# Kernel tuning notes

Hardware: AMD Instinct MI355X
Metric: run time of the kernel (lower is better)

Reference implementation:

```python
import jax, jax.numpy as jnp
import numpy as np

N = 100000   # nodes
E = 300000   # edges (avg degree ~3, molecular graphs)
DIN = 128    # input node features
H = 512      # hidden
OUT = 256    # out_channels
G = 4096     # number of graphs
EPS = 1e-5
SLOPE = 0.01  # LeakyReLU default negative slope
SELF_W = 2.0  # improved=True self-loop weight


def setup_inputs() -> dict:
    key = jax.random.key(0)
    ks = jax.random.split(key, 12)
    x = jax.random.normal(ks[0], (N, DIN), dtype=jnp.float32)
    edge_index = jax.random.randint(ks[1], (2, E), 0, N, dtype=jnp.int64)
    batch = jnp.sort(jax.random.randint(ks[2], (N,), 0, G, dtype=jnp.int64))
    s1 = 1.0 / np.sqrt(DIN)
    s2 = 1.0 / np.sqrt(H)
    return {
        "x": x,
        "edge_index": edge_index,
        "batch": batch,
        "W1": jax.random.normal(ks[3], (DIN, H), dtype=jnp.float32) * s1,
        "b1": jax.random.normal(ks[4], (H,), dtype=jnp.float32) * 0.01,
        "g1": jax.random.uniform(ks[5], (H,), dtype=jnp.float32, minval=0.5, maxval=1.5),
        "beta1": jax.random.normal(ks[6], (H,), dtype=jnp.float32) * 0.01,
        "W2": jax.random.normal(ks[7], (H, H), dtype=jnp.float32) * s2,
        "b2": jax.random.normal(ks[8], (H,), dtype=jnp.float32) * 0.01,
        "g2": jax.random.uniform(ks[9], (H,), dtype=jnp.float32, minval=0.5, maxval=1.5),
        "beta2": jax.random.normal(ks[10], (H,), dtype=jnp.float32) * 0.01,
        "Wf": jax.random.normal(ks[11], (H, OUT), dtype=jnp.float32) * s2,
        "bf": jnp.zeros((OUT,), dtype=jnp.float32),
    }


def _gcn_conv(x, W, b, row, col, n):
    # GCNConv(improved=True, add_self_loops=True, normalize=True), edge_weight=None
    h = x @ W                                   # [n, H]
    ones = jnp.ones(row.shape[0], dtype=h.dtype)
    deg = jax.ops.segment_sum(ones, col, num_segments=n) + SELF_W
    dinv = jax.lax.rsqrt(deg)                   # deg > 0 always (self-loop weight 2)
    norm = dinv[row] * dinv[col]                # [E]
    agg = jax.ops.segment_sum(h[row] * norm[:, None], col, num_segments=n)
    agg = agg + h * (SELF_W * dinv * dinv)[:, None]  # self-loop messages, no edge materialization
    return agg + b


def _bn(x, g, beta):
    # training-mode BatchNorm1d: biased batch stats
    mu = jnp.mean(x, axis=0)
    var = jnp.mean(jnp.square(x - mu), axis=0)
    return g * (x - mu) * jax.lax.rsqrt(var + EPS) + beta


def reference(x, edge_index, batch, W1, b1, g1, beta1, W2, b2, g2, beta2, Wf, bf):
    row, col = edge_index[0], edge_index[1]
    n = x.shape[0]
    h = _gcn_conv(x, W1, b1, row, col, n)
    h = jax.nn.leaky_relu(_bn(h, g1, beta1), SLOPE)
    # dropout is identity in eval mode
    h = _gcn_conv(h, W2, b2, row, col, n)
    h = jax.nn.leaky_relu(_bn(h, g2, beta2), SLOPE)
    pooled = jax.ops.segment_max(h, batch, num_segments=G)
    pooled = jnp.where(jnp.isfinite(pooled), pooled, 0.0)  # empty graphs -> 0 (torch_scatter fill)
    return pooled @ Wf + bf
```

## Files before the change

### kernel.cpp

```cpp
#include <hip/hip_runtime.h>
#include <hip/hip_bf16.h>

typedef __hip_bfloat16 bf16;
typedef __attribute__((ext_vector_type(8))) short short8;
typedef __attribute__((ext_vector_type(4))) float f32x4;

#define HDIM 512
#define SLOPE 0.01f
#define BN_EPS 1e-5f
#define STRIPES 8

__device__ inline float bf2f(short s) {
    unsigned u = ((unsigned)(unsigned short)s) << 16;
    return __builtin_bit_cast(float, u);
}
__device__ inline unsigned short f2bfbits(float v) {
    bf16 h = __float2bfloat16(v);
    return (unsigned short)__builtin_bit_cast(short, h);
}

struct EdgeRec { int src; float nm; };

__global__ void detect_types(const int* __restrict__ ei, const unsigned* __restrict__ xw,
                             int* __restrict__ flags, float* __restrict__ gpart) {
    __shared__ int nzhi, okbf;
    if (threadIdx.x == 0) { nzhi = 0; okbf = 0; }
    __syncthreads();
    int lo = 0, ok = 0;
    for (int i = threadIdx.x; i < 2048; i += 256)
        if (ei[2 * i + 1] != 0) lo++;
    for (int i = threadIdx.x; i < 1024; i += 256) {
        unsigned w = (xw[i] & 0xFFFFu) << 16;
        float av = fabsf(__builtin_bit_cast(float, w));
        if (av > 0.0009f && av < 64.0f) ok++;
    }
    for (int i = threadIdx.x; i < STRIPES * 2 * HDIM; i += 256) gpart[i] = 0.f;
    if (lo) atomicAdd(&nzhi, lo);
    if (ok) atomicAdd(&okbf, ok);
    __syncthreads();
    if (threadIdx.x == 0) {
        flags[0] = (nzhi == 0) ? 1 : 0;
        flags[1] = (okbf < 512) ? 1 : 0;
    }
}

__global__ void conv_all_idx(const int* __restrict__ ei, const int* __restrict__ batch,
                             int* __restrict__ ei32, int* __restrict__ batch32,
                             int* __restrict__ cnt, int e2, int n,
                             const int* __restrict__ flags) {
    int i = blockIdx.x * blockDim.x + threadIdx.x;
    int i64 = flags[0];
    if (i < e2) {
        int v = i64 ? (int)((const long long*)ei)[i] : ei[i];
        ei32[i] = v;
        if (i >= e2 / 2) atomicAdd(&cnt[v], 1);
    } else if (i < e2 + n) {
        int j = i - e2;
        batch32[j] = i64 ? (int)((const long long*)batch)[j] : batch[j];
    }
}

__global__ void wt_conv_all(const void* __restrict__ W1, const void* __restrict__ W2,
                            const void* __restrict__ Wf, const void* __restrict__ bf_,
                            bf16* __restrict__ W1T, bf16* __restrict__ W2T,
                            bf16* __restrict__ WfT, bf16* __restrict__ bfbf,
                            const int* __restrict__ flags) {
    const int S1 = 128 * 512, S2 = 512 * 512, S3 = 512 * 256;
    int idx = blockIdx.x * 256 + threadIdx.x;
    bool f32 = flags[1] != 0;
    if (idx < S1) {
        int nn = idx / 128, k = idx - nn * 128;
        float v = f32 ? ((const float*)W1)[(size_t)k * 512 + nn]
                      : __bfloat162float(((const bf16*)W1)[(size_t)k * 512 + nn]);
        W1T[idx] = __float2bfloat16(v);
    } else if (idx < S1 + S2) {
        int t = idx - S1;
        int nn = t / 512, k = t - nn * 512;
        float v = f32 ? ((const float*)W2)[(size_t)k * 512 + nn]
                      : __bfloat162float(((const bf16*)W2)[(size_t)k * 512 + nn]);
        W2T[t] = __float2bfloat16(v);
    } else if (idx < S1 + S2 + S3) {
        int t = idx - S1 - S2;
        int nn = t / 512, k = t - nn * 512;
        float v = f32 ? ((const float*)Wf)[(size_t)k * 256 + nn]
                      : __bfloat162float(((const bf16*)Wf)[(size_t)k * 256 + nn]);
        WfT[t] = __float2bfloat16(v);
    } else if (idx < S1 + S2 + S3 + 256) {
        int t = idx - S1 - S2 - S3;
        float v = f32 ? ((const float*)bf_)[t]
                      : __bfloat162float(((const bf16*)bf_)[t]);
        bfbf[t] = __float2bfloat16(v);
    }
}

__global__ __launch_bounds__(256) void scan_part(
    const int* __restrict__ counts, int* __restrict__ offsets,
    int* __restrict__ bsum, float* __restrict__ dinv, float* __restrict__ selfw,
    int n)
{
    __shared__ int s[512];
    int b = blockIdx.x;
    int base = b * 512;
    int t = threadIdx.x;
    int c0 = (base + t       < n) ? counts[base + t]       : 0;
    int c1 = (base + t + 256 < n) ? counts[base + t + 256] : 0;
    s[t] = c0; s[t + 256] = c1;
    if (base + t < n) {
        float d = (float)c0 + 2.0f;
        dinv[base + t] = rsqrtf(d);
        selfw[base + t] = 2.0f / d;
    }
    if (base + t + 256 < n) {
        float d = (float)c1 + 2.0f;
        dinv[base + t + 256] = rsqrtf(d);
        selfw[base + t + 256] = 2.0f / d;
    }

    int offset = 1;
    for (int d = 256; d > 0; d >>= 1) {
        __syncthreads();
        if (t < d) {
            int ai = offset * (2 * t + 1) - 1;
            int bi = offset * (2 * t + 2) - 1;
            s[bi] += s[ai];
        }
        offset <<= 1;
    }
    __syncthreads();
    if (t == 0) { bsum[b] = s[511]; s[511] = 0; }
    for (int d = 1; d < 512; d <<= 1) {
        offset >>= 1;
        __syncthreads();
        if (t < d) {
            int ai = offset * (2 * t + 1) - 1;
            int bi = offset * (2 * t + 2) - 1;
            int tmp = s[ai]; s[ai] = s[bi]; s[bi] += tmp;
        }
    }
    __syncthreads();
    if (base + t < n)       offsets[base + t]       = s[t];
    if (base + t + 256 < n) offsets[base + t + 256] = s[t + 256];
}

__global__ __launch_bounds__(1024) void scan_tops(int* __restrict__ bsum, int nb) {
    __shared__ int s[1024];
    int t = threadIdx.x;
    s[t] = (t < nb) ? bsum[t] : 0;
    __syncthreads();
    for (int off = 1; off < 1024; off <<= 1) {
        int v = (t >= off) ? s[t - off] : 0;
        __syncthreads();
        s[t] += v;
        __syncthreads();
    }
    if (t < nb) bsum[t] = (t == 0) ? 0 : s[t - 1];
}

__global__ __launch_bounds__(256) void scan_add(
    int* __restrict__ offsets, const int* __restrict__ bsum, int n, int e)
{
    int b = blockIdx.x;
    int base = b * 512;
    int add = bsum[b];
    int t = threadIdx.x;
    if (base + t < n)       offsets[base + t]       += add;
    if (base + t + 256 < n) offsets[base + t + 256] += add;
    if (b == 0 && t == 0) offsets[n] = e;
}

__global__ void scatter_edges(const int* __restrict__ rows, const int* __restrict__ cols,
                              const int* __restrict__ offsets, int* __restrict__ cursor,
                              const float* __restrict__ dinv,
                              EdgeRec* __restrict__ er, int e)
{
    int i = blockIdx.x * blockDim.x + threadIdx.x;
    if (i < e) {
        int d = cols[i];
        int r = rows[i];
        int pos = offsets[d] + atomicAdd(&cursor[d], 1);
        EdgeRec rec;
        rec.src = r;
        rec.nm = dinv[d] * dinv[r];
        er[pos] = rec;
    }
}

#define GEMM_STAGE(boff, kk)                                                             \
    {                                                                                    \
        _Pragma("unroll")                                                                \
        for (int i_ = 0; i_ < 2; i_++) {                                                 \
            int c_ = wave * 2 + i_;                                                      \
            const bf16* ga_ = A  + (size_t)(m0 + c_ * 16 + lrow) * K + (kk) + lcol;      \
            const bf16* gb_ = BT + (size_t)(n0 + c_ * 16 + lrow) * K + (kk) + lcol;      \
            __builtin_amdgcn_global_load_lds(                                            \
                (const __attribute__((address_space(1))) unsigned*)ga_,                  \
                (__attribute__((address_space(3))) unsigned*)(smem + (boff) + c_ * 512), \
                16, 0, 0);                                                               \
            __builtin_amdgcn_global_load_lds(                                            \
                (const __attribute__((address_space(1))) unsigned*)gb_,                  \
                (__attribute__((address_space(3))) unsigned*)(smem + 8192 + (boff) + c_ * 512), \
                16, 0, 0);                                                               \
        }                                                                                \
    }

#define GEMM_COMPUTE(boff)                                                               \
    {                                                                                    \
        short8 a[4], b[4];                                                               \
        _Pragma("unroll")                                                                \
        for (int mi2 = 0; mi2 < 4; mi2++)                                                \
            a[mi2] = *(const short8*)&smem[(boff) + (wm + mi2 * 16 + r) * 32 + aoff];    \
        _Pragma("unroll")                                                                \
        for (int ni = 0; ni < 4; ni++)                                                   \
            b[ni] = *(const short8*)&smem[8192 + (boff) + (wn + ni * 16 + r) * 32 + aoff]; \
        _Pragma("unroll")                                                                \
        for (int mi2 = 0; mi2 < 4; mi2++)                                                \
            _Pragma("unroll")                                                            \
            for (int ni = 0; ni < 4; ni++)                                               \
                acc[mi2][ni] = __builtin_amdgcn_mfma_f32_16x16x32_bf16(                  \
                    a[mi2], b[ni], acc[mi2][ni], 0, 0, 0);                               \
    }

template<bool STATS>
__global__ __launch_bounds__(256, 4) void gemm_m97(
    const bf16* __restrict__ A, const bf16* __restrict__ BT,
    void* __restrict__ C, const bf16* __restrict__ bias,
    int M, int K, int N, const int* __restrict__ cf32,
    float* __restrict__ gpart, int MB)
{
    __shared__ bf16 smem[16384];

    int NBN = N >> 7;
    int id = blockIdx.x;
    int grp = id / (8 * NBN);
    int loc = id - grp * 8 * NBN;
    int mi = loc & 7;
    int nblk = loc >> 3;
    int mblk = grp * 8 + mi;
    if (mblk >= MB) return;

    int tid = threadIdx.x;
    int wave = tid >> 6, lane = tid & 63, q = lane >> 4, r = lane & 15;
    int wm = (wave >> 1) * 64, wn = (wave & 1) * 64;
    int m0 = mblk * 128, n0 = nblk * 128;
    bool c32 = cf32 && *cf32;

    int lrow = lane >> 2;
    int lcol = (((lane & 3) ^ ((lane >> 3) & 3)) * 8);
    int aoff = (q ^ ((r >> 1) & 3)) * 8;

    f32x4 acc[4][4];
#pragma unroll
    for (int mi2 = 0; mi2 < 4; mi2++)
#pragma unroll
        for (int ni = 0; ni < 4; ni++)
            acc[mi2][ni] = {0.f, 0.f, 0.f, 0.f};

    const int nK = K >> 5;

    GEMM_STAGE(0, 0);

    int cur = 0;
    for (int t = 1; t < nK; ++t) {
        GEMM_STAGE(cur ^ 4096, t * 32);
        asm volatile("s_waitcnt vmcnt(4)" ::: "memory");
        __builtin_amdgcn_sched_barrier(0);
        __builtin_amdgcn_s_barrier();
        __builtin_amdgcn_sched_barrier(0);
        GEMM_COMPUTE(cur);
        asm volatile("s_waitcnt lgkmcnt(0)" ::: "memory");
        __builtin_amdgcn_sched_barrier(0);
        __builtin_amdgcn_s_barrier();
        __builtin_amdgcn_sched_barrier(0);
        cur ^= 4096;
    }
    asm volatile("s_waitcnt vmcnt(0)" ::: "memory");
    __builtin_amdgcn_sched_barrier(0);
    __builtin_amdgcn_s_barrier();
    __builtin_amdgcn_sched_barrier(0);
    GEMM_COMPUTE(cur);

    if (!c32) {
        __syncthreads();
#pragma unroll
        for (int mi2 = 0; mi2 < 4; mi2++) {
#pragma unroll
            for (int ni = 0; ni < 4; ni++) {
                int lc = wn + ni * 16 + r;
                float bv = bias ? __bfloat162float(bias[n0 + lc]) : 0.f;
#pragma unroll
                for (int reg = 0; reg < 4; reg++) {
                    int lr = wm + mi2 * 16 + q * 4 + reg;
                    int bo = ((lr << 8) + (lc << 1)) ^ (q << 5);
                    *(bf16*)((char*)smem + bo) = __float2bfloat16(acc[mi2][ni][reg] + bv);
                }
            }
        }
        __syncthreads();
#pragma unroll
        for (int pss = 0; pss < 8; pss++) {
            int off = pss * 4096 + tid * 16;
            int row = off >> 8;
            int cb = off & 255;
            int rb = cb ^ (((row >> 2) & 3) << 5);
            f32x4 v = *(const f32x4*)((const char*)smem + (row << 8) + rb);
            int gm = m0 + row;
            if (gm < M)
                *(f32x4*)((char*)C + (((size_t)gm * N + n0) << 1) + cb) = v;
        }
    } else {
#pragma unroll
        for (int mi2 = 0; mi2 < 4; mi2++) {
#pragma unroll
            for (int ni = 0; ni < 4; ni++) {
                int gn = n0 + wn + ni * 16 + r;
                float bv = bias ? __bfloat162float(bias[gn]) : 0.f;
#pragma unroll
                for (int reg = 0; reg < 4; reg++) {
                    int gm = m0 + wm + mi2 * 16 + q * 4 + reg;
                    if (gm < M)
                        ((float*)C)[(size_t)gm * N + gn] = acc[mi2][ni][reg] + bv;
                }
            }
        }
    }

    if constexpr (STATS) {
        float* base = gpart + (size_t)(mblk & (STRIPES - 1)) * 2 * HDIM;
#pragma unroll
        for (int ni = 0; ni < 4; ni++) {
            float cs = 0.f, cq = 0.f;
#pragma unroll
            for (int mi2 = 0; mi2 < 4; mi2++)
#pragma unroll
                for (int reg = 0; reg < 4; reg++) {
                    int gm = m0 + wm + mi2 * 16 + q * 4 + reg;
                    if (gm < M) {
                        float v = acc[mi2][ni][reg];
                        cs += v; cq += v * v;
                    }
                }
            cs += __shfl_xor(cs, 16, 64);
            cs += __shfl_xor(cs, 32, 64);
            cq += __shfl_xor(cq, 16, 64);
            cq += __shfl_xor(cq, 32, 64);
            if (q == 0) {
                int c = n0 + wn + ni * 16 + r;
                atomicAdd(&base[c], cs);
                atomicAdd(&base[HDIM + c], cq);
            }
        }
    }
}

#define AGG_DIN_BODY(LOADV)                                                            \
    int dst = gw;                                                                      \
    if (dst < n) {                                                                     \
        int s0 = offsets[dst], s1 = offsets[dst + 1];                                  \
        float sw = selfw[dst];                                                         \
        float h0, h1; LOADV(dst, h0, h1);                                              \
        while (dst < n) {                                                              \
            int nd = dst + nw;                                                         \
            int ns0 = 0, ns1 = 0; float nsw = 0.f, nh0 = 0.f, nh1 = 0.f;               \
            if (nd < n) {                                                              \
                ns0 = offsets[nd]; ns1 = offsets[nd + 1]; nsw = selfw[nd];             \
                LOADV(nd, nh0, nh1);                                                   \
            }                                                                          \
            float a0 = sw * h0, a1 = sw * h1;                                          \
            int p = s0;                                                                \
            for (; p + 3 < s1; p += 4) {                                               \
                EdgeRec e0 = er[p], e1 = er[p + 1], e2 = er[p + 2], e3 = er[p + 3];    \
                float x0, y0, x1, y1, x2, y2, x3, y3;                                  \
                LOADV(e0.src, x0, y0); LOADV(e1.src, x1, y1);                          \
                LOADV(e2.src, x2, y2); LOADV(e3.src, x3, y3);                          \
                a0 += e0.nm * x0 + e1.nm * x1 + e2.nm * x2 + e3.nm * x3;               \
                a1 += e0.nm * y0 + e1.nm * y1 + e2.nm * y2 + e3.nm * y3;               \
            }                                                                          \
            int rem = s1 - p;                                                          \
            if (rem > 0) {                                                             \
                EdgeRec e0 = er[p], e1 = e0, e2 = e0;                                  \
                if (rem > 1) e1 = er[p + 1];                                           \
                if (rem > 2) e2 = er[p + 2];                                           \
                float x0, y0, x1 = 0.f, y1 = 0.f, x2 = 0.f, y2 = 0.f;                  \
                LOADV(e0.src, x0, y0);                                                 \
                if (rem > 1) LOADV(e1.src, x1, y1);                                    \
                if (rem > 2) LOADV(e2.src, x2, y2);                                    \
                a0 += e0.nm * x0; a1 += e0.nm * y0;                                    \
                if (rem > 1) { a0 += e1.nm * x1; a1 += e1.nm * y1; }                   \
                if (rem > 2) { a0 += e2.nm * x2; a1 += e2.nm * y2; }                   \
            }                                                                          \
            ((unsigned*)out)[(size_t)dst * 64 + lane] =                                \
                (unsigned)f2bfbits(a0) | ((unsigned)f2bfbits(a1) << 16);               \
            dst = nd; s0 = ns0; s1 = ns1; sw = nsw; h0 = nh0; h1 = nh1;                \
        }                                                                              \
    }

#define LOADF32(idx, a, b) { float2 v_ = ((const float2*)x)[(size_t)(idx) * 64 + lane]; \
                             a = v_.x; b = v_.y; }
#define LOADBF(idx, a, b)  { unsigned u_ = ((const unsigned*)x)[(size_t)(idx) * 64 + lane]; \
                             a = bf2f((short)(u_ & 0xFFFF)); b = bf2f((short)(u_ >> 16)); }

__global__ __launch_bounds__(256) void agg_csr_din(
    const void* __restrict__ x, const int* __restrict__ offsets,
    const EdgeRec* __restrict__ er, const float* __restrict__ selfw,
    bf16* __restrict__ out, int n, const int* __restrict__ flags)
{
    int wave = threadIdx.x >> 6, lane = threadIdx.x & 63;
    int gw = blockIdx.x * 4 + wave;
    int nw = gridDim.x * 4;
    bool f32 = flags[1] != 0;
    if (f32) { AGG_DIN_BODY(LOADF32) } else { AGG_DIN_BODY(LOADBF) }
}

__device__ inline void bnlk8(const short8& v, const float* sc, const float* sh,
                             float* t) {
#pragma unroll
    for (int j = 0; j < 8; j++) {
        float u = sc[j] * bf2f(v[j]) + sh[j];
        t[j] = u > 0.f ? u : SLOPE * u;
    }
}

__global__ __launch_bounds__(256) void agg_csr_bn(
    const bf16* __restrict__ h, const int* __restrict__ offsets,
    const EdgeRec* __restrict__ er, const float* __restrict__ selfw,
    const float* __restrict__ scale, const float* __restrict__ shift,
    bf16* __restrict__ y, int n)
{
    int wave = threadIdx.x >> 6, lane = threadIdx.x & 63;
    int f0 = lane * 8;
    int gw = blockIdx.x * 4 + wave;
    int nw = gridDim.x * 4;

    float sc[8], sh[8];
#pragma unroll
    for (int j = 0; j < 8; j++) { sc[j] = scale[f0 + j]; sh[j] = shift[f0 + j]; }

    int dst = gw;
    if (dst >= n) return;
    int s0 = offsets[dst], s1 = offsets[dst + 1];
    float sw = selfw[dst];
    short8 hv = *(const short8*)(h + (size_t)dst * HDIM + f0);

    while (dst < n) {
        int nd = dst + nw;
        int ns0 = 0, ns1 = 0; float nsw = 0.f; short8 nhv = {};
        if (nd < n) {
            ns0 = offsets[nd]; ns1 = offsets[nd + 1]; nsw = selfw[nd];
            nhv = *(const short8*)(h + (size_t)nd * HDIM + f0);
        }

        float acc[8], t[8];
        bnlk8(hv, sc, sh, t);
#pragma unroll
        for (int j = 0; j < 8; j++) acc[j] = sw * t[j];

        int p = s0;
        for (; p + 3 < s1; p += 4) {
            EdgeRec e0 = er[p], e1 = er[p + 1], e2 = er[p + 2], e3 = er[p + 3];
            short8 v0 = *(const short8*)(h + (size_t)e0.src * HDIM + f0);
            short8 v1 = *(const short8*)(h + (size_t)e1.src * HDIM + f0);
            short8 v2 = *(const short8*)(h + (size_t)e2.src * HDIM + f0);
            short8 v3 = *(const short8*)(h + (size_t)e3.src * HDIM + f0);
            float t0[8], t1[8], t2[8], t3[8];
            bnlk8(v0, sc, sh, t0); bnlk8(v1, sc, sh, t1);
            bnlk8(v2, sc, sh, t2); bnlk8(v3, sc, sh, t3);
#pragma unroll
            for (int j = 0; j < 8; j++)
                acc[j] += e0.nm * t0[j] + e1.nm * t1[j] + e2.nm * t2[j] + e3.nm * t3[j];
        }
        int rem = s1 - p;
        if (rem > 0) {
            EdgeRec e0 = er[p], e1 = e0, e2 = e0;
            if (rem > 1) e1 = er[p + 1];
            if (rem > 2) e2 = er[p + 2];
            short8 v0 = *(const short8*)(h + (size_t)e0.src * HDIM + f0);
            short8 v1 = {}, v2 = {};
            if (rem > 1) v1 = *(const short8*)(h + (size_t)e1.src * HDIM + f0);
            if (rem > 2) v2 = *(const short8*)(h + (size_t)e2.src * HDIM + f0);
            float t0[8];
            bnlk8(v0, sc, sh, t0);
#pragma unroll
            for (int j = 0; j < 8; j++) acc[j] += e0.nm * t0[j];
            if (rem > 1) {
                float t1[8]; bnlk8(v1, sc, sh, t1);
#pragma unroll
                for (int j = 0; j < 8; j++) acc[j] += e1.nm * t1[j];
            }
            if (rem > 2) {
                float t2[8]; bnlk8(v2, sc, sh, t2);
#pragma unroll
                for (int j = 0; j < 8; j++) acc[j] += e2.nm * t2[j];
            }
        }

        short8 o;
#pragma unroll
        for (int j = 0; j < 8; j++) ((bf16*)&o)[j] = __float2bfloat16(acc[j]);
        *(short8*)(y + (size_t)dst * HDIM + f0) = o;

        dst = nd; s0 = ns0; s1 = ns1; sw = nsw; hv = nhv;
    }
}

__global__ void bn_final(float* __restrict__ gpart,
                         const void* __restrict__ gamma, const void* __restrict__ beta,
                         float* __restrict__ scale, float* __restrict__ shift,
                         float invN, const int* __restrict__ flags)
{
    int f = threadIdx.x;
    float s = 0.f, q = 0.f;
#pragma unroll
    for (int k = 0; k < STRIPES; k++) {
        s += gpart[(size_t)k * 2 * HDIM + f];
        q += gpart[(size_t)k * 2 * HDIM + HDIM + f];
        gpart[(size_t)k * 2 * HDIM + f] = 0.f;
        gpart[(size_t)k * 2 * HDIM + HDIM + f] = 0.f;
    }
    float g = flags[1] ? ((const float*)gamma)[f]
                       : __bfloat162float(((const bf16*)gamma)[f]);
    float b = flags[1] ? ((const float*)beta)[f]
                       : __bfloat162float(((const bf16*)beta)[f]);
    float mu = s * invN;
    float var = fmaxf(q * invN - mu * mu, 0.f);
    float inv = rsqrtf(var + BN_EPS);
    float sc = g * inv;
    scale[f] = sc;
    shift[f] = b - mu * sc;
}

__global__ __launch_bounds__(256) void pool_fused(
    const bf16* __restrict__ y, const int* __restrict__ batch,
    const float* __restrict__ scale, const float* __restrict__ shift,
    bf16* __restrict__ pooled, int n, int G)
{
    int wave = threadIdx.x >> 6, lane = threadIdx.x & 63;
    int g = blockIdx.x * 4 + wave;
    if (g >= G) return;
    int f0 = lane * 8;

    int lo = 0, hi = n;
    while (lo < hi) { int mid = (lo + hi) >> 1; if (batch[mid] < g) lo = mid + 1; else hi = mid; }
    int s = lo;
    hi = n;
    while (lo < hi) { int mid = (lo + hi) >> 1; if (batch[mid] <= g) lo = mid + 1; else hi = mid; }
    int e = lo;

    float mx[8], mn[8];
#pragma unroll
    for (int j = 0; j < 8; j++) { mx[j] = -3.0e38f; mn[j] = 3.0e38f; }

    int rr = s;
    for (; rr + 1 < e; rr += 2) {
        short8 v0 = *(const short8*)(y + (size_t)rr * HDIM + f0);
        short8 v1 = *(const short8*)(y + (size_t)(rr + 1) * HDIM + f0);
#pragma unroll
        for (int j = 0; j < 8; j++) {
            float a = bf2f(v0[j]), b = bf2f(v1[j]);
            mx[j] = fmaxf(mx[j], fmaxf(a, b));
            mn[j] = fminf(mn[j], fminf(a, b));
        }
    }
    if (rr < e) {
        short8 v0 = *(const short8*)(y + (size_t)rr * HDIM + f0);
#pragma unroll
        for (int j = 0; j < 8; j++) {
            float a = bf2f(v0[j]);
            mx[j] = fmaxf(mx[j], a);
            mn[j] = fminf(mn[j], a);
        }
    }

    short8 o;
#pragma unroll
    for (int j = 0; j < 8; j++) {
        float outv = 0.f;
        if (s < e) {
            float sc = scale[f0 + j];
            float t = sc * (sc >= 0.f ? mx[j] : mn[j]) + shift[f0 + j];
            outv = t > 0.f ? t : SLOPE * t;
        }
        ((bf16*)&o)[j] = __float2bfloat16(outv);
    }
    *(short8*)(pooled + (size_t)g * HDIM + f0) = o;
}

extern "C" void kernel_launch(void* const* d_in, const int* in_sizes, int n_in,
                              void* d_out, int out_size, void* d_ws, size_t ws_size,
                              hipStream_t stream)
{
    const void* x     = d_in[0];
    const int*  ei    = (const int*)d_in[1];
    const int*  batch = (const int*)d_in[2];

    const int N   = in_sizes[2];
    const int E   = in_sizes[1] / 2;
    const int DIN = 128;
    const int OUT = 256;
    const int G   = out_size / OUT;
    const int Mp  = (N + 127) & ~127;
    const int MB  = Mp / 128;
    const int MB8 = (MB + 7) & ~7;

    char* p = (char*)d_ws;
    bf16* B1     = (bf16*)p;  p += (size_t)Mp * HDIM * sizeof(bf16);
    bf16* B2     = (bf16*)p;  p += (size_t)Mp * HDIM * sizeof(bf16);
    bf16* Q      = (bf16*)p;  p += (size_t)Mp * DIN * sizeof(bf16);
    bf16* W1T    = (bf16*)p;  p += (size_t)HDIM * DIN * sizeof(bf16);
    bf16* W2T    = (bf16*)p;  p += (size_t)HDIM * HDIM * sizeof(bf16);
    bf16* WfT    = (bf16*)p;  p += (size_t)OUT * HDIM * sizeof(bf16);
    bf16* bfbf   = (bf16*)p;  p += 512 * sizeof(bf16);
    int* ei32    = (int*)p;   p += (size_t)2 * E * sizeof(int);
    int* batch32 = (int*)p;   p += (size_t)N * sizeof(int);
    float* dinv  = (float*)p; p += (size_t)N * sizeof(float);
    float* selfw = (float*)p; p += (size_t)N * sizeof(float);
    int* offsets = (int*)p;   p += (size_t)(N + 4) * sizeof(int);
    int* cursor  = (int*)p;   p += (size_t)N * sizeof(int);
    EdgeRec* er  = (EdgeRec*)p; p += (size_t)E * sizeof(EdgeRec);
    int* bsum    = (int*)p;   p += 1024 * sizeof(int);
    float* gpart = (float*)p; p += (size_t)STRIPES * 2 * HDIM * sizeof(float);
    float* sc1   = (float*)p; p += HDIM * sizeof(float);
    float* sh1   = (float*)p; p += HDIM * sizeof(float);
    float* sc2   = (float*)p; p += HDIM * sizeof(float);
    float* sh2   = (float*)p; p += HDIM * sizeof(float);
    int* flags   = (int*)p;   p += 4 * sizeof(int);

    detect_types<<<1, 256, 0, stream>>>(ei, (const unsigned*)x, flags, gpart);
    hipMemsetAsync(cursor, 0, (size_t)N * sizeof(int), stream);
    conv_all_idx<<<(2 * E + N + 255) / 256, 256, 0, stream>>>(
        ei, batch, ei32, batch32, cursor, 2 * E, N, flags);
    wt_conv_all<<<(128 * 512 + 512 * 512 + 512 * 256 + 256 + 255) / 256, 256, 0, stream>>>(
        d_in[3], d_in[7], d_in[11], d_in[12], W1T, W2T, WfT, bfbf, flags);

    const int* rows = ei32;
    const int* cols = ei32 + E;

    int nb = (N + 511) / 512;
    scan_part<<<nb, 256, 0, stream>>>(cursor, offsets, bsum, dinv, selfw, N);
    scan_tops<<<1, 1024, 0, stream>>>(bsum, nb);
    scan_add<<<nb, 256, 0, stream>>>(offsets, bsum, N, E);
    hipMemsetAsync(cursor, 0, (size_t)N * sizeof(int), stream);
    scatter_edges<<<(E + 255) / 256, 256, 0, stream>>>(rows, cols, offsets, cursor,
                                                       dinv, er, E);

    int gemm_blocks = MB8 * (HDIM / 128);

    agg_csr_din<<<2048, 256, 0, stream>>>(x, offsets, er, selfw, Q, N, flags);
    gemm_m97<true><<<gemm_blocks, 256, 0, stream>>>(
        Q, W1T, B2, nullptr, N, DIN, HDIM, nullptr, gpart, MB);
    bn_final<<<1, HDIM, 0, stream>>>(gpart, d_in[5], d_in[6], sc1, sh1, 1.0f / N, flags);

    agg_csr_bn<<<2048, 256, 0, stream>>>(B2, offsets, er, selfw, sc1, sh1, B1, N);
    gemm_m97<true><<<gemm_blocks, 256, 0, stream>>>(
        B1, W2T, B2, nullptr, N, HDIM, HDIM, nullptr, gpart, MB);
    bn_final<<<1, HDIM, 0, stream>>>(gpart, d_in[9], d_in[10], sc2, sh2, 1.0f / N, flags);

    pool_fused<<<(G + 3) / 4, 256, 0, stream>>>(B2, batch32, sc2, sh2, Q, N, G);
    gemm_m97<false><<<(G / 128) * (OUT / 128), 256, 0, stream>>>(
        Q, WfT, d_out, bfbf, G, HDIM, OUT, flags + 1, nullptr, G / 128);
}
```

Baseline: 431.4 us.

## Fuse segment max/min pooling into second GEMM epilogue, drop pre-BN activation write

The second GCN GEMM no longer writes its 100k x 512 bf16 output. Its epilogue instead reduces per-graph column max and min in shared memory and publishes them to global partial buffers, using float atomics only for graphs split across row tiles. A small finalize kernel then applies the BN affine (picking max or min by the sign of the scale) and LeakyReLU. Separately, index and weight conversion are merged into one launch, and the scan writes the cursor directly so a memset and an offset load are gone. The cost is an extra init pass over four G x H float buffers and LDS atomics in the GEMM epilogue.

```diff
diff --git a/kernel.cpp b/kernel.cpp
--- a/kernel.cpp
+++ b/kernel.cpp
@@ -17,6 +17,15 @@
 __device__ inline unsigned short f2bfbits(float v) {
     bf16 h = __float2bfloat16(v);
     return (unsigned short)__builtin_bit_cast(short, h);
+}
+
+__device__ inline void atomicMaxF(float* a, float v) {
+    if (v >= 0.f) atomicMax((int*)a, __float_as_int(v));
+    else          atomicMin((unsigned int*)a, __float_as_uint(v));
+}
+__device__ inline void atomicMinF(float* a, float v) {
+    if (v >= 0.f) atomicMin((int*)a, __float_as_int(v));
+    else          atomicMax((unsigned int*)a, __float_as_uint(v));
 }
 
 struct EdgeRec { int src; float nm; };
@@ -44,12 +53,18 @@
     }
 }
 
-__global__ void conv_all_idx(const int* __restrict__ ei, const int* __restrict__ batch,
-                             int* __restrict__ ei32, int* __restrict__ batch32,
-                             int* __restrict__ cnt, int e2, int n,
-                             const int* __restrict__ flags) {
-    int i = blockIdx.x * blockDim.x + threadIdx.x;
+__global__ void conv_wt_all(const int* __restrict__ ei, const int* __restrict__ batch,
+                            int* __restrict__ ei32, int* __restrict__ batch32,
+                            int* __restrict__ cnt, int e2, int n,
+                            const void* __restrict__ W1, const void* __restrict__ W2,
+                            const void* __restrict__ Wf, const void* __restrict__ bf_,
+                            bf16* __restrict__ W1T, bf16* __restrict__ W2T,
+                            bf16* __restrict__ WfT, bf16* __restrict__ bfbf,
+                            const int* __restrict__ flags) {
+    const int S1 = 128 * 512, S2 = 512 * 512, S3 = 512 * 256;
+    int i = blockIdx.x * 256 + threadIdx.x;
     int i64 = flags[0];
+    bool f32 = flags[1] != 0;
     if (i < e2) {
         int v = i64 ? (int)((const long long*)ei)[i] : ei[i];
         ei32[i] = v;
@@ -57,39 +72,31 @@
     } else if (i < e2 + n) {
         int j = i - e2;
         batch32[j] = i64 ? (int)((const long long*)batch)[j] : batch[j];
-    }
-}
-
-__global__ void wt_conv_all(const void* __restrict__ W1, const void* __restrict__ W2,
-                            const void* __restrict__ Wf, const void* __restrict__ bf_,
-                            bf16* __restrict__ W1T, bf16* __restrict__ W2T,
-                            bf16* __restrict__ WfT, bf16* __restrict__ bfbf,
-                            const int* __restrict__ flags) {
-    const int S1 = 128 * 512, S2 = 512 * 512, S3 = 512 * 256;
-    int idx = blockIdx.x * 256 + threadIdx.x;
-    bool f32 = flags[1] != 0;
-    if (idx < S1) {
-        int nn = idx / 128, k = idx - nn * 128;
-        float v = f32 ? ((const float*)W1)[(size_t)k * 512 + nn]
-                      : __bfloat162float(((const bf16*)W1)[(size_t)k * 512 + nn]);
-        W1T[idx] = __float2bfloat16(v);
-    } else if (idx < S1 + S2) {
-        int t = idx - S1;
-        int nn = t / 512, k = t - nn * 512;
-        float v = f32 ? ((const float*)W2)[(size_t)k * 512 + nn]
-                      : __bfloat162float(((const bf16*)W2)[(size_t)k * 512 + nn]);
-        W2T[t] = __float2bfloat16(v);
-    } else if (idx < S1 + S2 + S3) {
-        int t = idx - S1 - S2;
-        int nn = t / 512, k = t - nn * 512;
-        float v = f32 ? ((const float*)Wf)[(size_t)k * 256 + nn]
-                      : __bfloat162float(((const bf16*)Wf)[(size_t)k * 256 + nn]);
-        WfT[t] = __float2bfloat16(v);
-    } else if (idx < S1 + S2 + S3 + 256) {
-        int t = idx - S1 - S2 - S3;
-        float v = f32 ? ((const float*)bf_)[t]
-                      : __bfloat162float(((const bf16*)bf_)[t]);
-        bfbf[t] = __float2bfloat16(v);
+    } else {
+        int idx = i - e2 - n;
+        if (idx < S1) {
+            int nn = idx / 128, k = idx - nn * 128;
+            float v = f32 ? ((const float*)W1)[(size_t)k * 512 + nn]
+                          : __bfloat162float(((const bf16*)W1)[(size_t)k * 512 + nn]);
+            W1T[idx] = __float2bfloat16(v);
+        } else if (idx < S1 + S2) {
+            int t = idx - S1;
+            int nn = t / 512, k = t - nn * 512;
+            float v = f32 ? ((const float*)W2)[(size_t)k * 512 + nn]
+                          : __bfloat162float(((const bf16*)W2)[(size_t)k * 512 + nn]);
+            W2T[t] = __float2bfloat16(v);
+        } else if (idx < S1 + S2 + S3) {
+            int t = idx - S1 - S2;
+            int nn = t / 512, k = t - nn * 512;
+            float v = f32 ? ((const float*)Wf)[(size_t)k * 256 + nn]
+                          : __bfloat162float(((const bf16*)Wf)[(size_t)k * 256 + nn]);
+            WfT[t] = __float2bfloat16(v);
+        } else if (idx < S1 + S2 + S3 + 256) {
+            int t = idx - S1 - S2 - S3;
+            float v = f32 ? ((const float*)bf_)[t]
+                          : __bfloat162float(((const bf16*)bf_)[t]);
+            bfbf[t] = __float2bfloat16(v);
+        }
     }
 }
 
@@ -157,32 +164,61 @@
 }
 
 __global__ __launch_bounds__(256) void scan_add(
-    int* __restrict__ offsets, const int* __restrict__ bsum, int n, int e)
+    int* __restrict__ offsets, const int* __restrict__ bsum,
+    int* __restrict__ cursor, int n, int e)
 {
     int b = blockIdx.x;
     int base = b * 512;
     int add = bsum[b];
     int t = threadIdx.x;
-    if (base + t < n)       offsets[base + t]       += add;
-    if (base + t + 256 < n) offsets[base + t + 256] += add;
+    if (base + t < n) {
+        int v = offsets[base + t] + add;
+        offsets[base + t] = v; cursor[base + t] = v;
+    }
+    if (base + t + 256 < n) {
+        int v = offsets[base + t + 256] + add;
+        offsets[base + t + 256] = v; cursor[base + t + 256] = v;
+    }
     if (b == 0 && t == 0) offsets[n] = e;
 }
 
 __global__ void scatter_edges(const int* __restrict__ rows, const int* __restrict__ cols,
-                              const int* __restrict__ offsets, int* __restrict__ cursor,
-                              const float* __restrict__ dinv,
+                              int* __restrict__ cursor, const float* __restrict__ dinv,
                               EdgeRec* __restrict__ er, int e)
 {
     int i = blockIdx.x * blockDim.x + threadIdx.x;
     if (i < e) {
         int d = cols[i];
         int r = rows[i];
-        int pos = offsets[d] + atomicAdd(&cursor[d], 1);
+        int pos = atomicAdd(&cursor[d], 1);
         EdgeRec rec;
         rec.src = r;
         rec.nm = dinv[d] * dinv[r];
         er[pos] = rec;
     }
+}
+
+__global__ __launch_bounds__(256) void pool_init2(float* __restrict__ pS, int total, int gn) {
+    int i = blockIdx.x * 256 + threadIdx.x;
+    if (i < total) pS[i] = ((i / gn) & 1) ? 3.0e38f : -3.0e38f;
+}
+
+__global__ __launch_bounds__(256) void pool_fin2(
+    const float* __restrict__ pS, const float* __restrict__ scale,
+    const float* __restrict__ shift, bf16* __restrict__ outQ, int gn)
+{
+    int i = blockIdx.x * 256 + threadIdx.x;
+    if (i >= gn) return;
+    int c = i & (HDIM - 1);
+    float vmax = fmaxf(pS[i], pS[2 * (size_t)gn + i]);
+    float vmin = fminf(pS[(size_t)gn + i], pS[3 * (size_t)gn + i]);
+    float outv = 0.f;
+    if (vmax > -2.9e38f) {
+        float s = scale[c];
+        float t = s * (s >= 0.f ? vmax : vmin) + shift[c];
+        outv = t > 0.f ? t : SLOPE * t;
+    }
+    outQ[i] = __float2bfloat16(outv);
 }
 
 #define GEMM_STAGE(boff, kk)                                                             \
@@ -220,12 +256,13 @@
                     a[mi2], b[ni], acc[mi2][ni], 0, 0, 0);                               \
     }
 
-template<bool STATS>
+template<bool STATS, bool POOL>
 __global__ __launch_bounds__(256, 4) void gemm_m97(
     const bf16* __restrict__ A, const bf16* __restrict__ BT,
     void* __restrict__ C, const bf16* __restrict__ bias,
     int M, int K, int N, const int* __restrict__ cf32,
-    float* __restrict__ gpart, int MB)
+    float* __restrict__ gpart, int MB,
+    const int* __restrict__ batchp, float* __restrict__ pS, int gn_total)
 {
     __shared__ bf16 smem[16384];
 
@@ -279,48 +316,125 @@
     __builtin_amdgcn_sched_barrier(0);
     GEMM_COMPUTE(cur);
 
-    if (!c32) {
+    if constexpr (!POOL) {
+        if (!c32) {
+            __syncthreads();
+#pragma unroll
+            for (int mi2 = 0; mi2 < 4; mi2++) {
+#pragma unroll
+                for (int ni = 0; ni < 4; ni++) {
+                    int lc = wn + ni * 16 + r;
+                    float bv = bias ? __bfloat162float(bias[n0 + lc]) : 0.f;
+#pragma unroll
+                    for (int reg = 0; reg < 4; reg++) {
+                        int lr = wm + mi2 * 16 + q * 4 + reg;
+                        int bo = ((lr << 8) + (lc << 1)) ^ (q << 5);
+                        *(bf16*)((char*)smem + bo) = __float2bfloat16(acc[mi2][ni][reg] + bv);
+                    }
+                }
+            }
+            __syncthreads();
+#pragma unroll
+            for (int pss = 0; pss < 8; pss++) {
+                int off = pss * 4096 + tid * 16;
+                int row = off >> 8;
+                int cb = off & 255;
+                int rb = cb ^ (((row >> 2) & 3) << 5);
+                f32x4 v = *(const f32x4*)((const char*)smem + (row << 8) + rb);
+                int gm = m0 + row;
+                if (gm < M)
+                    *(f32x4*)((char*)C + (((size_t)gm * N + n0) << 1) + cb) = v;
+            }
+        } else {
+#pragma unroll
+            for (int mi2 = 0; mi2 < 4; mi2++) {
+#pragma unroll
+                for (int ni = 0; ni < 4; ni++) {
+                    int gn = n0 + wn + ni * 16 + r;
+                    float bv = bias ? __bfloat162float(bias[gn]) : 0.f;
+#pragma unroll
+                    for (int reg = 0; reg < 4; reg++) {
+                        int gm = m0 + wm + mi2 * 16 + q * 4 + reg;
+                        if (gm < M)
+                            ((float*)C)[(size_t)gm * N + gn] = acc[mi2][ni][reg] + bv;
+                    }
+                }
+            }
+        }
+    }
+
+    if constexpr (POOL) {
+        int batchv[16];
+#pragma unroll
+        for (int mi2 = 0; mi2 < 4; mi2++)
+#pragma unroll
+            for (int reg = 0; reg < 4; reg++) {
+                int gm = m0 + wm + mi2 * 16 + q * 4 + reg;
+                batchv[mi2 * 4 + reg] = (gm < M) ? batchp[gm] : -1;
+            }
+        int gfirst = batchp[m0];
+        int lastrow = (m0 + 127 < M) ? (m0 + 127) : (M - 1);
+        int glast = batchp[lastrow];
+        int ng = glast - gfirst + 1;
+        bool home0 = (m0 == 0) || (batchp[m0 - 1] < gfirst);
+        float* part  = (float*)smem;
+        float* s0max = pS;
+        float* s0min = pS + (size_t)gn_total;
+        float* s1max = pS + 2 * (size_t)gn_total;
+        float* s1min = pS + 3 * (size_t)gn_total;
         __syncthreads();
-#pragma unroll
-        for (int mi2 = 0; mi2 < 4; mi2++) {
+        for (int gbase = 0; gbase < ng; gbase += 32) {
+            int nwin = ng - gbase; if (nwin > 32) nwin = 32;
+            for (int i = tid; i < nwin * 256; i += 256)
+                part[i] = (i & 1) ? 3.0e38f : -3.0e38f;
+            __syncthreads();
 #pragma unroll
             for (int ni = 0; ni < 4; ni++) {
                 int lc = wn + ni * 16 + r;
-                float bv = bias ? __bfloat162float(bias[n0 + lc]) : 0.f;
-#pragma unroll
-                for (int reg = 0; reg < 4; reg++) {
-                    int lr = wm + mi2 * 16 + q * 4 + reg;
-                    int bo = ((lr << 8) + (lc << 1)) ^ (q << 5);
-                    *(bf16*)((char*)smem + bo) = __float2bfloat16(acc[mi2][ni][reg] + bv);
+                float cmax = 0.f, cmin = 0.f;
+                int curg = -1;
+#pragma unroll
+                for (int t2 = 0; t2 < 16; t2++) {
+                    int g2 = batchv[t2];
+                    float v = acc[t2 >> 2][ni][t2 & 3];
+                    if (g2 >= 0) {
+                        if (g2 != curg) {
+                            if (curg >= 0) {
+                                int gi = curg - gfirst - gbase;
+                                if (gi >= 0 && gi < nwin) {
+                                    atomicMaxF(&part[(gi * 128 + lc) * 2], cmax);
+                                    atomicMinF(&part[(gi * 128 + lc) * 2 + 1], cmin);
+                                }
+                            }
+                            curg = g2; cmax = v; cmin = v;
+                        } else {
+                            cmax = fmaxf(cmax, v); cmin = fminf(cmin, v);
+                        }
+                    }
                 }
-            }
-        }
-        __syncthreads();
-#pragma unroll
-        for (int pss = 0; pss < 8; pss++) {
-            int off = pss * 4096 + tid * 16;
-            int row = off >> 8;
-            int cb = off & 255;
-            int rb = cb ^ (((row >> 2) & 3) << 5);
-            f32x4 v = *(const f32x4*)((const char*)smem + (row << 8) + rb);
-            int gm = m0 + row;
-            if (gm < M)
-                *(f32x4*)((char*)C + (((size_t)gm * N + n0) << 1) + cb) = v;
-        }
-    } else {
-#pragma unroll
-        for (int mi2 = 0; mi2 < 4; mi2++) {
-#pragma unroll
-            for (int ni = 0; ni < 4; ni++) {
-                int gn = n0 + wn + ni * 16 + r;
-                float bv = bias ? __bfloat162float(bias[gn]) : 0.f;
-#pragma unroll
-                for (int reg = 0; reg < 4; reg++) {
-                    int gm = m0 + wm + mi2 * 16 + q * 4 + reg;
-                    if (gm < M)
-                        ((float*)C)[(size_t)gm * N + gn] = acc[mi2][ni][reg] + bv;
+                if (curg >= 0) {
+                    int gi = curg - gfirst - gbase;
+                    if (gi >= 0 && gi < nwin) {
+                        atomicMaxF(&part[(gi * 128 + lc) * 2], cmax);
+                        atomicMinF(&part[(gi * 128 + lc) * 2 + 1], cmin);
+                    }
                 }
             }
+            __syncthreads();
+            for (int i = tid; i < nwin * 256; i += 256) {
+                int cell = i >> 1;
+                int gi = cell >> 7, col = cell & 127;
+                int g2 = gfirst + gbase + gi;
+                float v = part[i];
+                size_t gidx = (size_t)g2 * N + n0 + col;
+                bool nh = (g2 == gfirst) && !home0;
+                if (i & 1) {
+                    if (nh) atomicMinF(&s1min[gidx], v); else s0min[gidx] = v;
+                } else {
+                    if (nh) atomicMaxF(&s1max[gidx], v); else s0max[gidx] = v;
+                }
+            }
+            __syncthreads();
         }
     }
 
@@ -528,62 +642,6 @@
     shift[f] = b - mu * sc;
 }
 
-__global__ __launch_bounds__(256) void pool_fused(
-    const bf16* __restrict__ y, const int* __restrict__ batch,
-    const float* __restrict__ scale, const float* __restrict__ shift,
-    bf16* __restrict__ pooled, int n, int G)
-{
-    int wave = threadIdx.x >> 6, lane = threadIdx.x & 63;
-    int g = blockIdx.x * 4 + wave;
-    if (g >= G) return;
-    int f0 = lane * 8;
-
-    int lo = 0, hi = n;
-    while (lo < hi) { int mid = (lo + hi) >> 1; if (batch[mid] < g) lo = mid + 1; else hi = mid; }
-    int s = lo;
-    hi = n;
-    while (lo < hi) { int mid = (lo + hi) >> 1; if (batch[mid] <= g) lo = mid + 1; else hi = mid; }
-    int e = lo;
-
-    float mx[8], mn[8];
-#pragma unroll
-    for (int j = 0; j < 8; j++) { mx[j] = -3.0e38f; mn[j] = 3.0e38f; }
-
-    int rr = s;
-    for (; rr + 1 < e; rr += 2) {
-        short8 v0 = *(const short8*)(y + (size_t)rr * HDIM + f0);
-        short8 v1 = *(const short8*)(y + (size_t)(rr + 1) * HDIM + f0);
-#pragma unroll
-        for (int j = 0; j < 8; j++) {
-            float a = bf2f(v0[j]), b = bf2f(v1[j]);
-            mx[j] = fmaxf(mx[j], fmaxf(a, b));
-            mn[j] = fminf(mn[j], fminf(a, b));
-        }
-    }
-    if (rr < e) {
-        short8 v0 = *(const short8*)(y + (size_t)rr * HDIM + f0);
-#pragma unroll
-        for (int j = 0; j < 8; j++) {
-            float a = bf2f(v0[j]);
-            mx[j] = fmaxf(mx[j], a);
-            mn[j] = fminf(mn[j], a);
-        }
-    }
-
-    short8 o;
-#pragma unroll
-    for (int j = 0; j < 8; j++) {
-        float outv = 0.f;
-        if (s < e) {
-            float sc = scale[f0 + j];
-            float t = sc * (sc >= 0.f ? mx[j] : mn[j]) + shift[f0 + j];
-            outv = t > 0.f ? t : SLOPE * t;
-        }
-        ((bf16*)&o)[j] = __float2bfloat16(outv);
-    }
-    *(short8*)(pooled + (size_t)g * HDIM + f0) = o;
-}
-
 extern "C" void kernel_launch(void* const* d_in, const int* in_sizes, int n_in,
                               void* d_out, int out_size, void* d_ws, size_t ws_size,
                               hipStream_t stream)
@@ -624,12 +682,17 @@
     float* sh2   = (float*)p; p += HDIM * sizeof(float);
     int* flags   = (int*)p;   p += 4 * sizeof(int);
 
+    float* pS = (float*)B2;
+    const int GN = G * HDIM;
+
     detect_types<<<1, 256, 0, stream>>>(ei, (const unsigned*)x, flags, gpart);
     hipMemsetAsync(cursor, 0, (size_t)N * sizeof(int), stream);
-    conv_all_idx<<<(2 * E + N + 255) / 256, 256, 0, stream>>>(
-        ei, batch, ei32, batch32, cursor, 2 * E, N, flags);
-    wt_conv_all<<<(128 * 512 + 512 * 512 + 512 * 256 + 256 + 255) / 256, 256, 0, stream>>>(
-        d_in[3], d_in[7], d_in[11], d_in[12], W1T, W2T, WfT, bfbf, flags);
+    {
+        const int WTOT = 128 * 512 + 512 * 512 + 512 * 256 + 256;
+        conv_wt_all<<<(2 * E + N + WTOT + 255) / 256, 256, 0, stream>>>(
+            ei, batch, ei32, batch32, cursor, 2 * E, N,
+            d_in[3], d_in[7], d_in[11], d_in[12], W1T, W2T, WfT, bfbf, flags);
+    }
 
     const int* rows = ei32;
     const int* cols = ei32 + E;
@@ -637,24 +700,26 @@
     int nb = (N + 511) / 512;
     scan_part<<<nb, 256, 0, stream>>>(cursor, offsets, bsum, dinv, selfw, N);
     scan_tops<<<1, 1024, 0, stream>>>(bsum, nb);
-    scan_add<<<nb, 256, 0, stream>>>(offsets, bsum, N, E);
-    hipMemsetAsync(cursor, 0, (size_t)N * sizeof(int), stream);
-    scatter_edges<<<(E + 255) / 256, 256, 0, stream>>>(rows, cols, offsets, cursor,
-                                                       dinv, er, E);
+    scan_add<<<nb, 256, 0, stream>>>(offsets, bsum, cursor, N, E);
+    scatter_edges<<<(E + 255) / 256, 256, 0, stream>>>(rows, cols, cursor, dinv, er, E);
 
     int gemm_blocks = MB8 * (HDIM / 128);
 
     agg_csr_din<<<2048, 256, 0, stream>>>(x, offsets, er, selfw, Q, N, flags);
-    gemm_m97<true><<<gemm_blocks, 256, 0, stream>>>(
-        Q, W1T, B2, nullptr, N, DIN, HDIM, nullptr, gpart, MB);
+    gemm_m97<true, false><<<gemm_blocks, 256, 0, stream>>>(
+        Q, W1T, B2, nullptr, N, DIN, HDIM, nullptr, gpart, MB,
+        nullptr, nullptr, 0);
     bn_final<<<1, HDIM, 0, stream>>>(gpart, d_in[5], d_in[6], sc1, sh1, 1.0f / N, flags);
 
     agg_csr_bn<<<2048, 256, 0, stream>>>(B2, offsets, er, selfw, sc1, sh1, B1, N);
-    gemm_m97<true><<<gemm_blocks, 256, 0, stream>>>(
-        B1, W2T, B2, nullptr, N, HDIM, HDIM, nullptr, gpart, MB);
+    pool_init2<<<(4 * GN + 255) / 256, 256, 0, stream>>>(pS, 4 * GN, GN);
+    gemm_m97<true, true><<<gemm_blocks, 256, 0, stream>>>(
+        B1, W2T, nullptr, nullptr, N, HDIM, HDIM, nullptr, gpart, MB,
+        batch32, pS, GN);
     bn_final<<<1, HDIM, 0, stream>>>(gpart, d_in[9], d_in[10], sc2, sh2, 1.0f / N, flags);
 
-    pool_fused<<<(G + 3) / 4, 256, 0, stream>>>(B2, batch32, sc2, sh2, Q, N, G);
-    gemm_m97<false><<<(G / 128) * (OUT / 128), 256, 0, stream>>>(
-        Q, WfT, d_out, bfbf, G, HDIM, OUT, flags + 1, nullptr, G / 128);
-}
+    pool_fin2<<<(GN + 255) / 256, 256, 0, stream>>>(pS, sc2, sh2, Q, GN);
+    gemm_m97<false, false><<<(G / 128) * (OUT / 128), 256, 0, stream>>>(
+        Q, WfT, d_out, bfbf, G, HDIM, OUT, flags + 1, nullptr, G / 128,
+        nullptr, nullptr, 0);
+}
```

Result: faster. 417.1 us (-3.3%).
